# Performance work log

Measured on AMD Instinct MI355X. Metric: run time of the kernel, lower is better.

## Reference

```python
import jax, jax.numpy as jnp
import numpy as np

EPS = 1e-5

def _ln(x, g, b):
    m = jnp.mean(x, axis=-1, keepdims=True)
    v = jnp.mean(jnp.square(x - m), axis=-1, keepdims=True)
    return (x - m) * jax.lax.rsqrt(v + EPS) * g + b

def setup_inputs() -> dict:
    key = jax.random.key(0)
    ks = jax.random.split(key, 20)
    B, F = 262144, 768
    sizes = [F, 512, 256, 128, 1]  # LN(d_in) -> Linear(d_in, d_out) per block
    inp = {"input": jax.random.normal(ks[0], (B, F), dtype=jnp.float32)}
    for i in range(4):
        din, dout = sizes[i], sizes[i + 1]
        inp[f"g{i}"] = jnp.ones((din,), dtype=jnp.float32)
        inp[f"b{i}"] = jnp.zeros((din,), dtype=jnp.float32)
        bound = 1.0 / np.sqrt(din)
        inp[f"W{i}"] = jax.random.uniform(ks[1 + 2 * i], (dout, din), dtype=jnp.float32, minval=-bound, maxval=bound)
        inp[f"c{i}"] = jax.random.uniform(ks[2 + 2 * i], (dout,), dtype=jnp.float32, minval=-bound, maxval=bound)
    return inp

def reference(input, g0, b0, W0, c0, g1, b1, W1, c1, g2, b2, W2, c2, g3, b3, W3, c3):
    x = input
    params = [(g0, b0, W0, c0), (g1, b1, W1, c1), (g2, b2, W2, c2), (g3, b3, W3, c3)]
    for i, (g, b, W, c) in enumerate(params):
        x = _ln(x, g, b)
        x = x @ W.T + c
        if i != 3:
            x = jax.nn.elu(x)
    return jnp.squeeze(x, axis=-1)  # [B]
```

## Files before the change

### kernel.cpp

```cpp
#include <hip/hip_runtime.h>
#include <hip/hip_fp16.h>
#include <math.h>

typedef _Float16 half_t;
typedef half_t half2_t __attribute__((ext_vector_type(2)));
typedef half_t half4_t __attribute__((ext_vector_type(4)));
typedef half_t half8_t __attribute__((ext_vector_type(8)));
typedef float f32x4 __attribute__((ext_vector_type(4)));

#define LN_EPS 1e-5f
#define FDOT2(a, b, c) __builtin_amdgcn_fdot2((a), (b), (c), false)

__global__ void pack_weights(const float* __restrict__ W0, const float* __restrict__ g0,
                             const float* __restrict__ W1, const float* __restrict__ g1,
                             const float* __restrict__ W2, const float* __restrict__ g2,
                             half_t* __restrict__ ws) {
    int sid = blockIdx.x * 256 + threadIdx.x;
    const float* W; const float* g; int K, T, off;
    if (sid < 49152)      { W = W0; g = g0; K = 768; T = 24; off = 0; }
    else if (sid < 65536) { W = W1; g = g1; K = 512; T = 16; off = 49152; sid -= 49152; }
    else if (sid < 69632) { W = W2; g = g2; K = 256; T = 8;  off = 65536; sid -= 65536; }
    else return;
    const int l   = sid & 63;
    const int t   = (sid >> 6) % T;
    const int cbg = (sid >> 6) / T;
    const int n   = (l & 15) + 16 * cbg;
    const int k0  = 32 * t + 8 * (l >> 4);
    const float* src = W + (size_t)n * K + k0;
    const float* gs  = g + k0;
    half8_t v;
    #pragma unroll
    for (int jq = 0; jq < 8; jq++) v[jq] = (half_t)(src[jq] * gs[jq]);
    *(half8_t*)(ws + (size_t)(off + sid) * 8) = v;
}

__global__ void fold_bias(const float* __restrict__ W0, const float* __restrict__ g0,
                          const float* __restrict__ b0, const float* __restrict__ c0,
                          const float* __restrict__ W1, const float* __restrict__ g1,
                          const float* __restrict__ b1, const float* __restrict__ c1,
                          const float* __restrict__ W2, const float* __restrict__ g2,
                          const float* __restrict__ b2, const float* __restrict__ c2,
                          const float* __restrict__ W3, const float* __restrict__ g3,
                          const float* __restrict__ b3, const float* __restrict__ c3,
                          float* __restrict__ f) {
    const int gw   = (blockIdx.x * 256 + threadIdx.x) >> 6;
    const int lane = threadIdx.x & 63;
    if (gw == 896) {
        float s = 0.f, cb_ = 0.f;
        for (int k = lane; k < 128; k += 64) {
            const float wg = W3[k] * g3[k];
            f[1792 + k] = wg;
            s += wg; cb_ += W3[k] * b3[k];
        }
        #pragma unroll
        for (int m = 1; m < 64; m <<= 1) { s += __shfl_xor(s, m); cb_ += __shfl_xor(cb_, m); }
        if (lane == 0) { f[1920] = s; f[1921] = cb_ + c3[0]; }
        return;
    }
    const float *W, *g, *b, *cc; int K, n; float *sf, *cf;
    if (gw < 512)      { W = W0; g = g0; b = b0; cc = c0; K = 768; n = gw;       sf = f;        cf = f + 512; }
    else if (gw < 768) { W = W1; g = g1; b = b1; cc = c1; K = 512; n = gw - 512; sf = f + 1024; cf = f + 1280; }
    else if (gw < 896) { W = W2; g = g2; b = b2; cc = c2; K = 256; n = gw - 768; sf = f + 1536; cf = f + 1664; }
    else return;
    const float* Wr = W + (size_t)n * K;
    float s = 0.f, cb_ = 0.f;
    for (int k = lane; k < K; k += 64) { const float wg = Wr[k] * g[k]; s += wg; cb_ += Wr[k] * b[k]; }
    #pragma unroll
    for (int m = 1; m < 64; m <<= 1) { s += __shfl_xor(s, m); cb_ += __shfl_xor(cb_, m); }
    if (lane == 0) { sf[n] = s; cf[n] = cb_ + cc[n]; }
}

__global__ __launch_bounds__(512, 2)
void fused_mlp(const float* __restrict__ x_in,
               const half_t* __restrict__ W0p, const half_t* __restrict__ W1p,
               const half_t* __restrict__ W2p, const float* __restrict__ f,
               float* __restrict__ out)
{
    __shared__ half_t xreg[32768];
    __shared__ half_t stg2[16384];
    __shared__ float rmA[64], rsA[64], rmB[64], rsB[64];
    __shared__ float ps[8][64], pq[8][64];
    __shared__ half2_t w3h[64];

    const int tid  = threadIdx.x;
    const int lane = tid & 63;
    const int wv   = tid >> 6;
    const int grp  = lane >> 4;
    const int cl   = lane & 15;
    const int row  = tid >> 3;
    const int jj   = tid & 7;
    const int rbw  = row >> 4;
    const long r0  = (long)blockIdx.x * 128;
    const float* xrA = x_in + (r0 + row) * 768;
    const float* xrB = xrA + 64 * 768;

    const float* s0f = f;        const float* c0f = f + 512;
    const float* s1f = f + 1024; const float* c1f = f + 1280;
    const float* s2f = f + 1536; const float* c2f = f + 1664;
    const half2_t one2 = {(half_t)1.f, (half_t)1.f};

    if (tid < 64) {
        half2_t w; w[0] = (half_t)f[1792 + 2 * tid]; w[1] = (half_t)f[1793 + 2 * tid];
        w3h[tid] = w;
    }

    float sA = 0.f, ssA = 0.f, sB = 0.f, ssB = 0.f;
    f32x4 vb[4];
    f32x4 acc0[4][4];
    f32x4 acc1[4][2];
    f32x4 acc2[4];

    auto zacc0 = [&]() {
        #pragma unroll
        for (int rb = 0; rb < 4; rb++)
            #pragma unroll
            for (int cb = 0; cb < 4; cb++) acc0[rb][cb] = 0.f;
    };

    auto stage_load = [&](const float* xr, int c) {
        const float* xp = xr + 128 * c + 4 * jj;
        #pragma unroll
        for (int i = 0; i < 4; i++)
            vb[i] = __builtin_nontemporal_load((const f32x4*)(xp + 32 * i));
    };
    auto stage_write = [&](int c, float& s_, float& ss_) {
        half_t* fb = stg2 + 8192 * (c & 1);
        const int hg = jj >> 1, jo = 4 * (jj & 1);
        #pragma unroll
        for (int i = 0; i < 4; i++) {
            const f32x4 v = vb[i];
            half2_t h01; h01[0] = (half_t)v[0]; h01[1] = (half_t)v[1];
            half2_t h23; h23[0] = (half_t)v[2]; h23[1] = (half_t)v[3];
            s_  = FDOT2(h01, one2, s_);  s_  = FDOT2(h23, one2, s_);
            ss_ = FDOT2(h01, h01, ss_);  ss_ = FDOT2(h23, h23, ss_);
            half4_t hv; hv[0] = h01[0]; hv[1] = h01[1]; hv[2] = h23[0]; hv[3] = h23[1];
            *(half4_t*)(&fb[((i * 4 + rbw) * 64 + ((row & 15) + 16 * hg)) * 8 + jo]) = hv;
        }
    };
    auto ln0_fin = [&](float& s_, float& ss_, float* rm, float* rs) {
        s_  += __shfl_xor(s_, 1);  s_  += __shfl_xor(s_, 2);  s_  += __shfl_xor(s_, 4);
        ss_ += __shfl_xor(ss_, 1); ss_ += __shfl_xor(ss_, 2); ss_ += __shfl_xor(ss_, 4);
        if (jj == 0) {
            const float mm = s_ * (1.f / 768.f);
            rm[row] = mm;
            rs[row] = 1.f / sqrtf(ss_ * (1.f / 768.f) - mm * mm + LN_EPS);
        }
    };
    auto gemm0c = [&](int c) {
        const half_t* fb = stg2 + 8192 * (c & 1);
        const half_t* wp = W0p + (size_t)(4 * wv * 24 + 4 * c) * 512 + lane * 8;
        half8_t bA[4], bB[4];
        #pragma unroll
        for (int cb = 0; cb < 4; cb++) bA[cb] = *(const half8_t*)(wp + cb * 12288);
        #pragma unroll
        for (int tt = 0; tt < 4; tt++) {
            half8_t* cur = (tt & 1) ? bB : bA;
            half8_t* nxt = (tt & 1) ? bA : bB;
            if (tt < 3) {
                #pragma unroll
                for (int cb = 0; cb < 4; cb++)
                    nxt[cb] = *(const half8_t*)(wp + (tt + 1) * 512 + cb * 12288);
            }
            half8_t af[4];
            #pragma unroll
            for (int rb = 0; rb < 4; rb++)
                af[rb] = *(const half8_t*)(&fb[((tt * 4 + rb) * 64 + lane) * 8]);
            #pragma unroll
            for (int cb = 0; cb < 4; cb++)
                #pragma unroll
                for (int rb = 0; rb < 4; rb++)
                    acc0[rb][cb] = __builtin_amdgcn_mfma_f32_16x16x32_f16(af[rb], cur[cb], acc0[rb][cb], 0, 0, 0);
        }
    };
    auto ep0 = [&](const float* rm0, const float* rs0) {
        float sv[4], cv[4];
        #pragma unroll
        for (int cb = 0; cb < 4; cb++) {
            const int c = cl + 16 * (4 * wv + cb);
            sv[cb] = s0f[c]; cv[cb] = c0f[c];
        }
        #pragma unroll
        for (int rb = 0; rb < 4; rb++)
            #pragma unroll
            for (int v = 0; v < 4; v++) {
                const int r = 16 * rb + 4 * grp + v;
                const float rm = rm0[r], rr = rs0[r];
                float a_ = 0.f, q_ = 0.f;
                #pragma unroll
                for (int cb = 0; cb < 4; cb++) {
                    float y = rr * (acc0[rb][cb][v] - rm * sv[cb]) + cv[cb];
                    y = y > 0.f ? y : (__expf(y) - 1.f);
                    acc0[rb][cb][v] = y;
                    a_ += y; q_ += y * y;
                }
                a_ += __shfl_xor(a_, 1); a_ += __shfl_xor(a_, 2); a_ += __shfl_xor(a_, 4); a_ += __shfl_xor(a_, 8);
                q_ += __shfl_xor(q_, 1); q_ += __shfl_xor(q_, 2); q_ += __shfl_xor(q_, 4); q_ += __shfl_xor(q_, 8);
                if (cl == 0) { ps[wv][r] = a_; pq[wv][r] = q_; }
            }
        #pragma unroll
        for (int cb = 0; cb < 4; cb++) {
            const int c = cl + 16 * (4 * wv + cb);
            const int t = c >> 5, j = c & 7, sc = 16 * ((c >> 3) & 3);
            #pragma unroll
            for (int rb = 0; rb < 4; rb++)
                #pragma unroll
                for (int v = 0; v < 4; v++)
                    xreg[((t * 4 + rb) * 64 + (4 * grp + v + sc)) * 8 + j] = (half_t)acc0[rb][cb][v];
        }
    };
    auto combine = [&](float* rm, float* rs, float inv) {
        if (tid < 64) {
            float a_ = 0.f, q_ = 0.f;
            #pragma unroll
            for (int w = 0; w < 8; w++) { a_ += ps[w][tid]; q_ += pq[w][tid]; }
            const float mm = a_ * inv;
            rm[tid] = mm;
            rs[tid] = 1.f / sqrtf(q_ * inv - mm * mm + LN_EPS);
        }
    };
    auto gemm1 = [&]() {
        #pragma unroll
        for (int rb = 0; rb < 4; rb++) { acc1[rb][0] = 0.f; acc1[rb][1] = 0.f; }
        const half_t* wp = W1p + (size_t)(2 * wv * 16) * 512 + lane * 8;
        half8_t bA[2], bB[2];
        bA[0] = *(const half8_t*)(wp);
        bA[1] = *(const half8_t*)(wp + 8192);
        #pragma unroll
        for (int t = 0; t < 16; t++) {
            half8_t* cur = (t & 1) ? bB : bA;
            half8_t* nxt = (t & 1) ? bA : bB;
            if (t < 15) {
                nxt[0] = *(const half8_t*)(wp + (t + 1) * 512);
                nxt[1] = *(const half8_t*)(wp + (t + 1) * 512 + 8192);
            }
            half8_t af[4];
            #pragma unroll
            for (int rb = 0; rb < 4; rb++)
                af[rb] = *(const half8_t*)(&xreg[((t * 4 + rb) * 64 + lane) * 8]);
            #pragma unroll
            for (int cb = 0; cb < 2; cb++)
                #pragma unroll
                for (int rb = 0; rb < 4; rb++)
                    acc1[rb][cb] = __builtin_amdgcn_mfma_f32_16x16x32_f16(af[rb], cur[cb], acc1[rb][cb], 0, 0, 0);
        }
    };
    auto ep1 = [&](const float* rm1, const float* rs1) {
        float sv[2], cv[2];
        #pragma unroll
        for (int cb = 0; cb < 2; cb++) {
            const int c = cl + 16 * (2 * wv + cb);
            sv[cb] = s1f[c]; cv[cb] = c1f[c];
        }
        #pragma unroll
        for (int rb = 0; rb < 4; rb++)
            #pragma unroll
            for (int v = 0; v < 4; v++) {
                const int r = 16 * rb + 4 * grp + v;
                const float rm = rm1[r], rr = rs1[r];
                float a_ = 0.f, q_ = 0.f;
                #pragma unroll
                for (int cb = 0; cb < 2; cb++) {
                    float y = rr * (acc1[rb][cb][v] - rm * sv[cb]) + cv[cb];
                    y = y > 0.f ? y : (__expf(y) - 1.f);
                    acc1[rb][cb][v] = y;
                    a_ += y; q_ += y * y;
                }
                a_ += __shfl_xor(a_, 1); a_ += __shfl_xor(a_, 2); a_ += __shfl_xor(a_, 4); a_ += __shfl_xor(a_, 8);
                q_ += __shfl_xor(q_, 1); q_ += __shfl_xor(q_, 2); q_ += __shfl_xor(q_, 4); q_ += __shfl_xor(q_, 8);
                if (cl == 0) { ps[wv][r] = a_; pq[wv][r] = q_; }
            }
        #pragma unroll
        for (int cb = 0; cb < 2; cb++) {
            const int c = cl + 16 * (2 * wv + cb);
            const int t = c >> 5, j = c & 7, sc = 16 * ((c >> 3) & 3);
            #pragma unroll
            for (int rb = 0; rb < 4; rb++)
                #pragma unroll
                for (int v = 0; v < 4; v++)
                    xreg[((t * 4 + rb) * 64 + (4 * grp + v + sc)) * 8 + j] = (half_t)acc1[rb][cb][v];
        }
    };
    auto gemm2 = [&]() {
        #pragma unroll
        for (int rb = 0; rb < 4; rb++) acc2[rb] = 0.f;
        const half_t* wp = W2p + (size_t)(wv * 8) * 512 + lane * 8;
        half8_t bA = *(const half8_t*)(wp);
        #pragma unroll
        for (int t = 0; t < 8; t++) {
            const half8_t cur = bA;
            if (t < 7) bA = *(const half8_t*)(wp + (t + 1) * 512);
            half8_t af[4];
            #pragma unroll
            for (int rb = 0; rb < 4; rb++)
                af[rb] = *(const half8_t*)(&xreg[((t * 4 + rb) * 64 + lane) * 8]);
            #pragma unroll
            for (int rb = 0; rb < 4; rb++)
                acc2[rb] = __builtin_amdgcn_mfma_f32_16x16x32_f16(af[rb], cur, acc2[rb], 0, 0, 0);
        }
    };
    auto ep2 = [&](const float* rm2, const float* rs2) {
        const int c2i = cl + 16 * wv;
        const float sv = s2f[c2i], cv = c2f[c2i];
        #pragma unroll
        for (int rb = 0; rb < 4; rb++)
            #pragma unroll
            for (int v = 0; v < 4; v++) {
                const int r = 16 * rb + 4 * grp + v;
                const float rm = rm2[r], rr = rs2[r];
                float y = rr * (acc2[rb][v] - rm * sv) + cv;
                y = y > 0.f ? y : (__expf(y) - 1.f);
                xreg[r * 136 + c2i] = (half_t)y;
            }
    };
    auto lastout = [&](long rbase) {
        float s_ = 0.f, q_ = 0.f, d_ = 0.f;
        #pragma unroll
        for (int u = 0; u < 2; u++) {
            const int cb = jj * 16 + 8 * u;
            const int wi = cb >> 1;
            const half8_t h = *(const half8_t*)(xreg + row * 136 + cb);
            half2_t p0 = {h[0], h[1]}, p1 = {h[2], h[3]}, p2 = {h[4], h[5]}, p3 = {h[6], h[7]};
            s_ = FDOT2(p0, one2, s_); s_ = FDOT2(p1, one2, s_);
            s_ = FDOT2(p2, one2, s_); s_ = FDOT2(p3, one2, s_);
            q_ = FDOT2(p0, p0, q_);   q_ = FDOT2(p1, p1, q_);
            q_ = FDOT2(p2, p2, q_);   q_ = FDOT2(p3, p3, q_);
            d_ = FDOT2(p0, w3h[wi], d_);     d_ = FDOT2(p1, w3h[wi + 1], d_);
            d_ = FDOT2(p2, w3h[wi + 2], d_); d_ = FDOT2(p3, w3h[wi + 3], d_);
        }
        s_ += __shfl_xor(s_, 1); s_ += __shfl_xor(s_, 2); s_ += __shfl_xor(s_, 4);
        q_ += __shfl_xor(q_, 1); q_ += __shfl_xor(q_, 2); q_ += __shfl_xor(q_, 4);
        d_ += __shfl_xor(d_, 1); d_ += __shfl_xor(d_, 2); d_ += __shfl_xor(d_, 4);
        if (jj == 0) {
            const float mm = s_ * (1.f / 128.f);
            const float rs = 1.f / sqrtf(q_ * (1.f / 128.f) - mm * mm + LN_EPS);
            out[rbase + row] = rs * (d_ - mm * f[1920]) + f[1921];
        }
    };

    zacc0();
    stage_load(xrA, 0); stage_write(0, sA, ssA);
    __syncthreads();
    #pragma unroll 1
    for (int c = 0; c < 6; c++) {
        if (c < 5) stage_load(xrA, c + 1);
        gemm0c(c);
        if (c < 5) stage_write(c + 1, sA, ssA);
        if (c == 4) ln0_fin(sA, ssA, rmA, rsA);
        __syncthreads();
    }

    stage_load(xrB, 0);
    ep0(rmA, rsA);
    stage_write(0, sB, ssB);
    __syncthreads();
    stage_load(xrB, 1);
    combine(rmA, rsA, 1.f / 512.f);
    zacc0();
    gemm1();
    gemm0c(0);
    stage_write(1, sB, ssB);
    __syncthreads();
    stage_load(xrB, 2);
    ep1(rmA, rsA);
    gemm0c(1);
    stage_write(2, sB, ssB);
    __syncthreads();
    stage_load(xrB, 3);
    combine(rmA, rsA, 1.f / 256.f);
    gemm2();
    gemm0c(2);
    stage_write(3, sB, ssB);
    __syncthreads();
    stage_load(xrB, 4);
    ep2(rmA, rsA);
    gemm0c(3);
    stage_write(4, sB, ssB);
    __syncthreads();
    stage_load(xrB, 5);
    lastout(r0);
    gemm0c(4);
    stage_write(5, sB, ssB);
    ln0_fin(sB, ssB, rmB, rsB);
    __syncthreads();
    gemm0c(5);
    __syncthreads();

    ep0(rmB, rsB);
    __syncthreads();
    combine(rmB, rsB, 1.f / 512.f);
    gemm1();
    __syncthreads();
    ep1(rmB, rsB);
    __syncthreads();
    combine(rmB, rsB, 1.f / 256.f);
    gemm2();
    __syncthreads();
    ep2(rmB, rsB);
    __syncthreads();
    lastout(r0 + 64);
}

extern "C" void kernel_launch(void* const* d_in, const int* in_sizes, int n_in,
                              void* d_out, int out_size, void* d_ws, size_t ws_size,
                              hipStream_t stream) {
    const float* x  = (const float*)d_in[0];
    const float* g0 = (const float*)d_in[1];
    const float* b0 = (const float*)d_in[2];
    const float* W0 = (const float*)d_in[3];
    const float* c0 = (const float*)d_in[4];
    const float* g1 = (const float*)d_in[5];
    const float* b1 = (const float*)d_in[6];
    const float* W1 = (const float*)d_in[7];
    const float* c1 = (const float*)d_in[8];
    const float* g2 = (const float*)d_in[9];
    const float* b2 = (const float*)d_in[10];
    const float* W2 = (const float*)d_in[11];
    const float* c2 = (const float*)d_in[12];
    const float* g3 = (const float*)d_in[13];
    const float* b3 = (const float*)d_in[14];
    const float* W3 = (const float*)d_in[15];
    const float* c3 = (const float*)d_in[16];

    half_t* ws = (half_t*)d_ws;
    float*  f  = (float*)(ws + 557056);

    pack_weights<<<272, 256, 0, stream>>>(W0, g0, W1, g1, W2, g2, ws);
    fold_bias<<<225, 256, 0, stream>>>(W0, g0, b0, c0, W1, g1, b1, c1,
                                       W2, g2, b2, c2, W3, g3, b3, c3, f);

    const int nrows = in_sizes[0] / 768;
    fused_mlp<<<nrows / 128, 512, 0, stream>>>(
        x, ws, ws + 393216, ws + 524288, f, (float*)d_out);
}
```

Baseline: 482.4 us.

## Convert fused MLP to persistent software-pipelined loop over 64-row tiles

Replaces the two-tile-per-block schedule with a persistent kernel of 256 blocks that each loop over many 64-row tiles. Layer-0 GEMM and input streaming for tile i run alongside the later layers and output of tile i-1. This spreads the pipeline prologue and epilogue across all tiles, so the serial tail of later layers no longer runs without overlapping loads. In exchange it uses a fixed grid of 256 (one block per CU on a 256-CU part, where launch bounds allowed two), which reduces occupancy, and it assumes the row count divides evenly.

```diff
diff --git a/kernel.cpp b/kernel.cpp
--- a/kernel.cpp
+++ b/kernel.cpp
@@ -74,11 +74,12 @@
 void fused_mlp(const float* __restrict__ x_in,
                const half_t* __restrict__ W0p, const half_t* __restrict__ W1p,
                const half_t* __restrict__ W2p, const float* __restrict__ f,
-               float* __restrict__ out)
+               float* __restrict__ out, int ntiles)
 {
     __shared__ half_t xreg[32768];
     __shared__ half_t stg2[16384];
-    __shared__ float rmA[64], rsA[64], rmB[64], rsB[64];
+    __shared__ float rm0[64], rs0[64];
+    __shared__ float rmT[64], rsT[64];
     __shared__ float ps[8][64], pq[8][64];
     __shared__ half2_t w3h[64];
 
@@ -90,9 +91,7 @@
     const int row  = tid >> 3;
     const int jj   = tid & 7;
     const int rbw  = row >> 4;
-    const long r0  = (long)blockIdx.x * 128;
-    const float* xrA = x_in + (r0 + row) * 768;
-    const float* xrB = xrA + 64 * 768;
+    const long tile0 = (long)blockIdx.x * ntiles;
 
     const float* s0f = f;        const float* c0f = f + 512;
     const float* s1f = f + 1024; const float* c1f = f + 1280;
@@ -104,7 +103,7 @@
         w3h[tid] = w;
     }
 
-    float sA = 0.f, ssA = 0.f, sB = 0.f, ssB = 0.f;
+    float sS = 0.f, ssS = 0.f;
     f32x4 vb[4];
     f32x4 acc0[4][4];
     f32x4 acc1[4][2];
@@ -116,14 +115,13 @@
             #pragma unroll
             for (int cb = 0; cb < 4; cb++) acc0[rb][cb] = 0.f;
     };
-
     auto stage_load = [&](const float* xr, int c) {
         const float* xp = xr + 128 * c + 4 * jj;
         #pragma unroll
         for (int i = 0; i < 4; i++)
             vb[i] = __builtin_nontemporal_load((const f32x4*)(xp + 32 * i));
     };
-    auto stage_write = [&](int c, float& s_, float& ss_) {
+    auto stage_write = [&](int c) {
         half_t* fb = stg2 + 8192 * (c & 1);
         const int hg = jj >> 1, jo = 4 * (jj & 1);
         #pragma unroll
@@ -131,20 +129,21 @@
             const f32x4 v = vb[i];
             half2_t h01; h01[0] = (half_t)v[0]; h01[1] = (half_t)v[1];
             half2_t h23; h23[0] = (half_t)v[2]; h23[1] = (half_t)v[3];
-            s_  = FDOT2(h01, one2, s_);  s_  = FDOT2(h23, one2, s_);
-            ss_ = FDOT2(h01, h01, ss_);  ss_ = FDOT2(h23, h23, ss_);
+            sS  = FDOT2(h01, one2, sS);  sS  = FDOT2(h23, one2, sS);
+            ssS = FDOT2(h01, h01, ssS);  ssS = FDOT2(h23, h23, ssS);
             half4_t hv; hv[0] = h01[0]; hv[1] = h01[1]; hv[2] = h23[0]; hv[3] = h23[1];
             *(half4_t*)(&fb[((i * 4 + rbw) * 64 + ((row & 15) + 16 * hg)) * 8 + jo]) = hv;
         }
     };
-    auto ln0_fin = [&](float& s_, float& ss_, float* rm, float* rs) {
-        s_  += __shfl_xor(s_, 1);  s_  += __shfl_xor(s_, 2);  s_  += __shfl_xor(s_, 4);
-        ss_ += __shfl_xor(ss_, 1); ss_ += __shfl_xor(ss_, 2); ss_ += __shfl_xor(ss_, 4);
+    auto ln0_fin = [&]() {
+        sS  += __shfl_xor(sS, 1);  sS  += __shfl_xor(sS, 2);  sS  += __shfl_xor(sS, 4);
+        ssS += __shfl_xor(ssS, 1); ssS += __shfl_xor(ssS, 2); ssS += __shfl_xor(ssS, 4);
         if (jj == 0) {
-            const float mm = s_ * (1.f / 768.f);
-            rm[row] = mm;
-            rs[row] = 1.f / sqrtf(ss_ * (1.f / 768.f) - mm * mm + LN_EPS);
-        }
+            const float mm = sS * (1.f / 768.f);
+            rm0[row] = mm;
+            rs0[row] = 1.f / sqrtf(ssS * (1.f / 768.f) - mm * mm + LN_EPS);
+        }
+        sS = 0.f; ssS = 0.f;
     };
     auto gemm0c = [&](int c) {
         const half_t* fb = stg2 + 8192 * (c & 1);
@@ -172,7 +171,7 @@
                     acc0[rb][cb] = __builtin_amdgcn_mfma_f32_16x16x32_f16(af[rb], cur[cb], acc0[rb][cb], 0, 0, 0);
         }
     };
-    auto ep0 = [&](const float* rm0, const float* rs0) {
+    auto ep0 = [&]() {
         float sv[4], cv[4];
         #pragma unroll
         for (int cb = 0; cb < 4; cb++) {
@@ -208,14 +207,14 @@
                     xreg[((t * 4 + rb) * 64 + (4 * grp + v + sc)) * 8 + j] = (half_t)acc0[rb][cb][v];
         }
     };
-    auto combine = [&](float* rm, float* rs, float inv) {
+    auto combine = [&](float inv) {
         if (tid < 64) {
             float a_ = 0.f, q_ = 0.f;
             #pragma unroll
             for (int w = 0; w < 8; w++) { a_ += ps[w][tid]; q_ += pq[w][tid]; }
             const float mm = a_ * inv;
-            rm[tid] = mm;
-            rs[tid] = 1.f / sqrtf(q_ * inv - mm * mm + LN_EPS);
+            rmT[tid] = mm;
+            rsT[tid] = 1.f / sqrtf(q_ * inv - mm * mm + LN_EPS);
         }
     };
     auto gemm1 = [&]() {
@@ -244,7 +243,7 @@
                     acc1[rb][cb] = __builtin_amdgcn_mfma_f32_16x16x32_f16(af[rb], cur[cb], acc1[rb][cb], 0, 0, 0);
         }
     };
-    auto ep1 = [&](const float* rm1, const float* rs1) {
+    auto ep1 = [&]() {
         float sv[2], cv[2];
         #pragma unroll
         for (int cb = 0; cb < 2; cb++) {
@@ -256,7 +255,7 @@
             #pragma unroll
             for (int v = 0; v < 4; v++) {
                 const int r = 16 * rb + 4 * grp + v;
-                const float rm = rm1[r], rr = rs1[r];
+                const float rm = rmT[r], rr = rsT[r];
                 float a_ = 0.f, q_ = 0.f;
                 #pragma unroll
                 for (int cb = 0; cb < 2; cb++) {
@@ -298,7 +297,7 @@
                 acc2[rb] = __builtin_amdgcn_mfma_f32_16x16x32_f16(af[rb], cur, acc2[rb], 0, 0, 0);
         }
     };
-    auto ep2 = [&](const float* rm2, const float* rs2) {
+    auto ep2 = [&]() {
         const int c2i = cl + 16 * wv;
         const float sv = s2f[c2i], cv = c2f[c2i];
         #pragma unroll
@@ -306,7 +305,7 @@
             #pragma unroll
             for (int v = 0; v < 4; v++) {
                 const int r = 16 * rb + 4 * grp + v;
-                const float rm = rm2[r], rr = rs2[r];
+                const float rm = rmT[r], rr = rsT[r];
                 float y = rr * (acc2[rb][v] - rm * sv) + cv;
                 y = y > 0.f ? y : (__expf(y) - 1.f);
                 xreg[r * 136 + c2i] = (half_t)y;
@@ -337,67 +336,41 @@
         }
     };
 
-    zacc0();
-    stage_load(xrA, 0); stage_write(0, sA, ssA);
-    __syncthreads();
     #pragma unroll 1
-    for (int c = 0; c < 6; c++) {
-        if (c < 5) stage_load(xrA, c + 1);
-        gemm0c(c);
-        if (c < 5) stage_write(c + 1, sA, ssA);
-        if (c == 4) ln0_fin(sA, ssA, rmA, rsA);
+    for (int i = 0; i <= ntiles; i++) {
+        const bool hasS = (i < ntiles);
+        const bool hasT = (i > 0);
+        const float* xr = x_in + (size_t)(tile0 + i) * 49152 + (size_t)row * 768;
+
+        if (hasS) stage_load(xr, 0);
+        if (hasT) ep0();
+        if (hasS) stage_write(0);
+        __syncthreads();
+        if (hasS) stage_load(xr, 1);
+        if (hasT) combine(1.f / 512.f);
+        zacc0();
+        if (hasT) gemm1();
+        if (hasS) { gemm0c(0); stage_write(1); }
+        __syncthreads();
+        if (hasS) stage_load(xr, 2);
+        if (hasT) ep1();
+        if (hasS) { gemm0c(1); stage_write(2); }
+        __syncthreads();
+        if (hasS) stage_load(xr, 3);
+        if (hasT) { combine(1.f / 256.f); gemm2(); }
+        if (hasS) { gemm0c(2); stage_write(3); }
+        __syncthreads();
+        if (hasS) stage_load(xr, 4);
+        if (hasT) ep2();
+        if (hasS) { gemm0c(3); stage_write(4); }
+        __syncthreads();
+        if (hasS) stage_load(xr, 5);
+        if (hasT) lastout((tile0 + i - 1) * 64);
+        if (hasS) { gemm0c(4); stage_write(5); ln0_fin(); }
+        __syncthreads();
+        if (hasS) gemm0c(5);
         __syncthreads();
     }
-
-    stage_load(xrB, 0);
-    ep0(rmA, rsA);
-    stage_write(0, sB, ssB);
-    __syncthreads();
-    stage_load(xrB, 1);
-    combine(rmA, rsA, 1.f / 512.f);
-    zacc0();
-    gemm1();
-    gemm0c(0);
-    stage_write(1, sB, ssB);
-    __syncthreads();
-    stage_load(xrB, 2);
-    ep1(rmA, rsA);
-    gemm0c(1);
-    stage_write(2, sB, ssB);
-    __syncthreads();
-    stage_load(xrB, 3);
-    combine(rmA, rsA, 1.f / 256.f);
-    gemm2();
-    gemm0c(2);
-    stage_write(3, sB, ssB);
-    __syncthreads();
-    stage_load(xrB, 4);
-    ep2(rmA, rsA);
-    gemm0c(3);
-    stage_write(4, sB, ssB);
-    __syncthreads();
-    stage_load(xrB, 5);
-    lastout(r0);
-    gemm0c(4);
-    stage_write(5, sB, ssB);
-    ln0_fin(sB, ssB, rmB, rsB);
-    __syncthreads();
-    gemm0c(5);
-    __syncthreads();
-
-    ep0(rmB, rsB);
-    __syncthreads();
-    combine(rmB, rsB, 1.f / 512.f);
-    gemm1();
-    __syncthreads();
-    ep1(rmB, rsB);
-    __syncthreads();
-    combine(rmB, rsB, 1.f / 256.f);
-    gemm2();
-    __syncthreads();
-    ep2(rmB, rsB);
-    __syncthreads();
-    lastout(r0 + 64);
 }
 
 extern "C" void kernel_launch(void* const* d_in, const int* in_sizes, int n_in,
@@ -428,7 +401,8 @@
     fold_bias<<<225, 256, 0, stream>>>(W0, g0, b0, c0, W1, g1, b1, c1,
                                        W2, g2, b2, c2, W3, g3, b3, c3, f);
 
-    const int nrows = in_sizes[0] / 768;
-    fused_mlp<<<nrows / 128, 512, 0, stream>>>(
-        x, ws, ws + 393216, ws + 524288, f, (float*)d_out);
+    const int nrows  = in_sizes[0] / 768;
+    const int ntiles = (nrows / 64) / 256;
+    fused_mlp<<<256, 512, 0, stream>>>(
+        x, ws, ws + 393216, ws + 524288, f, (float*)d_out, ntiles);
 }
```

Result: slower. 891.5 us (+84.8%).
